# Optimization experiments

Measured on AMD Instinct MI355X. Metric: run time of the kernel, lower is better.

Reference implementation:

```python
import jax, jax.numpy as jnp
import numpy as np

B, H, W, D, C = 2, 16, 16, 16, 128
UNITS = 128
BN_EPS = 1e-3  # keras BatchNormalization default epsilon


def setup_inputs() -> dict:
    key = jax.random.key(0)
    ks = jax.random.split(key, 12)
    lim = np.sqrt(3.0 / C)  # VarianceScaling(1.0, fan_avg, uniform)
    inp = {
        "x": jax.random.normal(ks[0], (B, H, W, D, C), dtype=jnp.float32),
        "gamma": jnp.ones((C,), jnp.float32),
        "beta": jnp.zeros((C,), jnp.float32),
        "moving_mean": jax.random.normal(ks[1], (C,), jnp.float32) * 0.1,
        "moving_var": jnp.ones((C,), jnp.float32) + 0.1 * jax.random.uniform(ks[2], (C,)),
        "Wq": jax.random.uniform(ks[3], (C, UNITS), jnp.float32, -lim, lim),
        "bq": jnp.zeros((UNITS,), jnp.float32),
        "Wk": jax.random.uniform(ks[4], (C, UNITS), jnp.float32, -lim, lim),
        "bk": jnp.zeros((UNITS,), jnp.float32),
        "Wv": jax.random.uniform(ks[5], (C, UNITS), jnp.float32, -lim, lim),
        "bv": jnp.zeros((UNITS,), jnp.float32),
        # proj uses kernel_init(0.0) -> effectively ~0; use tiny scale to keep grads nonzero
        "Wp": jax.random.uniform(ks[6], (UNITS, UNITS), jnp.float32, -1e-5, 1e-5),
        "bp": jnp.zeros((UNITS,), jnp.float32),
    }
    return inp


def reference(x, gamma, beta, moving_mean, moving_var, Wq, bq, Wk, bk, Wv, bv, Wp, bp):
    # BatchNormalization (inference mode): per-channel affine normalization
    xn = (x - moving_mean) * jax.lax.rsqrt(moving_var + BN_EPS) * gamma + beta
    b, h, w, d, c = xn.shape
    n = h * w * d
    scale = jnp.asarray(UNITS, jnp.float32) ** -0.5
    q = (xn @ Wq + bq).reshape(b, n, UNITS)
    k = (xn @ Wk + bk).reshape(b, n, UNITS)
    v = (xn @ Wv + bv).reshape(b, n, UNITS)
    # full self-attention over flattened 3D spatial dims: [b, n, n] scores
    attn = jax.nn.softmax(jnp.einsum('bnc,bmc->bnm', q, k) * scale, axis=-1)
    proj = jnp.einsum('bnm,bmc->bnc', attn, v).reshape(b, h, w, d, UNITS)
    proj = proj @ Wp + bp
    return xn + proj
```

## Files before the change

### kernel.cpp

```cpp
#include <hip/hip_runtime.h>
#include <hip/hip_bf16.h>

using bh8     = __attribute__((ext_vector_type(8))) short;
using floatx4 = __attribute__((ext_vector_type(4))) float;
using uintx2  = __attribute__((ext_vector_type(2))) unsigned;

#define MFMA16 __builtin_amdgcn_mfma_f32_16x16x32_bf16

__device__ __forceinline__ float b2f(short s) {
    union { unsigned u; float f; } v; v.u = ((unsigned)(unsigned short)s) << 16; return v.f;
}
__device__ __forceinline__ short f2b(float f) {
    union { float f; unsigned u; } v; v.f = f;
    unsigned r = (v.u + 0x7fffu + ((v.u >> 16) & 1u)) >> 16;
    return (short)r;
}
__device__ __forceinline__ unsigned pk2(float a, float b) {
    union { __hip_bfloat162 h; unsigned u; } v;
    v.h = __float22bfloat162_rn(make_float2(a, b));
    return v.u;
}
__device__ __forceinline__ float ldf(const void* p, int i, bool f32) {
    return f32 ? ((const float*)p)[i] : b2f(((const short*)p)[i]);
}
__device__ __forceinline__ bool detect_f32(const void* gamma) {
    return ((*(const unsigned*)gamma) & 0xFFFFu) == 0u;
}
__device__ __forceinline__ void gl2lds16(const short* g, short* l) {
    __builtin_amdgcn_global_load_lds(
        (const __attribute__((address_space(1))) void*)g,
        (__attribute__((address_space(3))) void*)l, 16, 0, 0);
}

#define LDW 136

__global__ __launch_bounds__(256) void k_bn_qkv(
    const void* __restrict__ xp,
    const void* __restrict__ gp, const void* __restrict__ bep,
    const void* __restrict__ mmp, const void* __restrict__ mvp,
    const void* __restrict__ Wqp, const void* __restrict__ bqp,
    const void* __restrict__ Wkp, const void* __restrict__ bkp,
    const void* __restrict__ Wvp, const void* __restrict__ bvp,
    short* __restrict__ Qo, short* __restrict__ Ko, short* __restrict__ Vt)
{
    __shared__ float sS[128], sT[128];
    __shared__ __align__(16) short Wt[128 * LDW];
    const bool f32 = detect_f32(gp);
    const int tid = threadIdx.x, wave = tid >> 6, lane = tid & 63;
    const int lq = lane >> 4, lr = lane & 15;
    const int g = blockIdx.x >> 6;
    const int tile = blockIdx.x & 63;
    const int row0 = tile * 128 + wave * 32;

    if (tid < 128) {
        float ga = ldf(gp, tid, f32), be = ldf(bep, tid, f32);
        float mm = ldf(mmp, tid, f32), mv = ldf(mvp, tid, f32);
        float s = ga * rsqrtf(mv + 1e-3f);
        sS[tid] = s;
        sT[tid] = be - mm * s;
    }

    const void* W  = (g == 0) ? Wqp : ((g == 1) ? Wkp : Wvp);
    const void* bb = (g == 0) ? bqp : ((g == 1) ? bkp : bvp);

    if (f32) {
        for (int it = 0; it < 16; ++it) {
            int f = (it * 256 + tid) * 4;
            int c = f >> 7, u = f & 127;
            floatx4 wv = *(const floatx4*)((const float*)W + f);
            #pragma unroll
            for (int jj = 0; jj < 4; ++jj) {
                int j = (jj + (tid >> 1)) & 3;
                Wt[(u + j) * LDW + c] = f2b(wv[j]);
            }
        }
    } else {
        for (int it = 0; it < 8; ++it) {
            int f = (it * 256 + tid) * 8;
            int c = f >> 7, u = f & 127;
            bh8 wv = *(const bh8*)((const short*)W + f);
            #pragma unroll
            for (int jj = 0; jj < 8; ++jj) {
                int j = (jj + tid) & 7;
                Wt[(u + j) * LDW + c] = wv[j];
            }
        }
    }
    __syncthreads();

    bh8 a[2][4];
    #pragma unroll
    for (int rt = 0; rt < 2; ++rt)
        #pragma unroll
        for (int ks = 0; ks < 4; ++ks) {
            int c0 = ks * 32 + lq * 8;
            floatx4 s0 = *(const floatx4*)(&sS[c0]), s1 = *(const floatx4*)(&sS[c0 + 4]);
            floatx4 t0 = *(const floatx4*)(&sT[c0]), t1 = *(const floatx4*)(&sT[c0 + 4]);
            bh8 af;
            if (f32) {
                const float* xr = (const float*)xp + (size_t)(row0 + rt * 16 + lr) * 128 + c0;
                floatx4 x0 = *(const floatx4*)xr, x1 = *(const floatx4*)(xr + 4);
                #pragma unroll
                for (int j = 0; j < 4; ++j) {
                    af[j]     = f2b(x0[j] * s0[j] + t0[j]);
                    af[j + 4] = f2b(x1[j] * s1[j] + t1[j]);
                }
            } else {
                bh8 xv = *(const bh8*)((const short*)xp + (size_t)(row0 + rt * 16 + lr) * 128 + c0);
                #pragma unroll
                for (int j = 0; j < 4; ++j) {
                    af[j]     = f2b(b2f(xv[j]) * s0[j] + t0[j]);
                    af[j + 4] = f2b(b2f(xv[j + 4]) * s1[j] + t1[j]);
                }
            }
            a[rt][ks] = af;
        }

    floatx4 acc[2][8] = {};
    #pragma unroll
    for (int ks = 0; ks < 4; ++ks)
        #pragma unroll
        for (int t = 0; t < 8; ++t) {
            bh8 b = *(const bh8*)(&Wt[(t * 16 + lr) * LDW + ks * 32 + lq * 8]);
            #pragma unroll
            for (int rt = 0; rt < 2; ++rt)
                acc[rt][t] = MFMA16(a[rt][ks], b, acc[rt][t], 0, 0, 0);
        }

    if (g < 2) {
        #pragma unroll
        for (int t = 0; t < 8; ++t) {
            int u = t * 16 + lr;
            float bias = ldf(bb, u, f32);
            #pragma unroll
            for (int rt = 0; rt < 2; ++rt)
                #pragma unroll
                for (int r = 0; r < 4; ++r) {
                    int grow = row0 + rt * 16 + lq * 4 + r;
                    short vb = f2b(acc[rt][t][r] + bias);
                    if (g == 0) Qo[(size_t)grow * 128 + u] = vb;
                    else        Ko[(size_t)grow * 128 + u] = vb;
                }
        }
    } else {
        __syncthreads();
        short* sVt = Wt;
        #pragma unroll
        for (int t = 0; t < 8; ++t) {
            int u = t * 16 + lr;
            float bias = ldf(bb, u, f32);
            #pragma unroll
            for (int rt = 0; rt < 2; ++rt)
                #pragma unroll
                for (int r = 0; r < 4; ++r) {
                    int n = wave * 32 + rt * 16 + lq * 4 + r;
                    sVt[u * LDW + n] = f2b(acc[rt][t][r] + bias);
                }
        }
        __syncthreads();
        int u = tid >> 1, nh = tid & 1;
        int grow0 = tile * 128 + nh * 64;
        int bsb = grow0 >> 12, nn = grow0 & 4095;
        short* dst = Vt + (size_t)bsb * 128 * 4096 + (size_t)u * 4096 + nn;
        #pragma unroll
        for (int j = 0; j < 8; ++j)
            *(bh8*)(dst + j * 8) = *(const bh8*)(&sVt[u * LDW + nh * 64 + j * 8]);
    }
}

#define PLDA 40

__global__ __launch_bounds__(256, 2) void k_attn(
    const short* __restrict__ Qg, const short* __restrict__ Kg,
    const short* __restrict__ Vtg, short* __restrict__ Op,
    float* __restrict__ Lq)
{
    __shared__ __align__(16) short sK[2][32 * 128];
    __shared__ __align__(16) short sV[2][128 * 32];
    __shared__ __align__(16) short sP[4][32 * PLDA];

    const int tid = threadIdx.x, wave = tid >> 6, lane = tid & 63;
    const int lq = lane >> 4, lr = lane & 15;
    const int qt = blockIdx.x >> 3, kq = blockIdx.x & 7;
    const int mq = qt * 128, bs = mq >> 12, key0q = kq * 512;
    const short* Kb = Kg + (size_t)bs * 4096 * 128;
    const short* Vb = Vtg + (size_t)bs * 128 * 4096;
    const int qrow0 = mq + wave * 32;

    bh8 aq[2][4];
    #pragma unroll
    for (int rt = 0; rt < 2; ++rt)
        #pragma unroll
        for (int ks = 0; ks < 4; ++ks)
            aq[rt][ks] = *(const bh8*)(Qg + (size_t)(qrow0 + rt * 16 + lr) * 128 + ks * 32 + lq * 8);

    const int kKey = lane >> 4, kCh = lane & 15;
    const int vU   = lane >> 2, vCh = lane & 3;

    floatx4 accO[2][8] = {};
    float lsum[2] = {};
    const float c2 = 0.12751743f;
    const float m2 = 11.541560f;
    short* Pw = &sP[wave][0];

    #pragma unroll
    for (int rd = 0; rd < 2; ++rd) {
        int key = wave * 8 + rd * 4 + kKey;
        gl2lds16(Kb + (size_t)(key0q + key) * 128 + ((kCh ^ (key & 7)) << 3),
                 &sK[0][(wave * 8 + rd * 4) * 128]);
    }
    #pragma unroll
    for (int rd = 0; rd < 2; ++rd) {
        int u = wave * 32 + rd * 16 + vU;
        gl2lds16(Vb + (size_t)u * 4096 + key0q + ((vCh ^ ((u >> 1) & 3)) << 3),
                 &sV[0][(wave * 32 + rd * 16) * 32]);
    }
    __syncthreads();

    for (int it = 0; it < 16; ++it) {
        const int p = it & 1;
        if (it < 15) {
            const int key1 = key0q + (it + 1) * 32;
            #pragma unroll
            for (int rd = 0; rd < 2; ++rd) {
                int key = wave * 8 + rd * 4 + kKey;
                gl2lds16(Kb + (size_t)(key1 + key) * 128 + ((kCh ^ (key & 7)) << 3),
                         &sK[p ^ 1][(wave * 8 + rd * 4) * 128]);
            }
            #pragma unroll
            for (int rd = 0; rd < 2; ++rd) {
                int u = wave * 32 + rd * 16 + vU;
                gl2lds16(Vb + (size_t)u * 4096 + key1 + ((vCh ^ ((u >> 1) & 3)) << 3),
                         &sV[p ^ 1][(wave * 32 + rd * 16) * 32]);
            }
        }

        const short* sKp = &sK[p][0];
        const short* sVp = &sV[p][0];

        floatx4 s[2][2];
        #pragma unroll
        for (int rt = 0; rt < 2; ++rt)
            #pragma unroll
            for (int t = 0; t < 2; ++t)
                s[rt][t] = floatx4{};
        #pragma unroll
        for (int t = 0; t < 2; ++t)
            #pragma unroll
            for (int ks = 0; ks < 4; ++ks) {
                bh8 kf = *(const bh8*)(&sKp[(t * 16 + lr) * 128 +
                                            (((ks * 4 + lq) ^ (lr & 7)) << 3)]);
                #pragma unroll
                for (int rt = 0; rt < 2; ++rt)
                    s[rt][t] = MFMA16(kf, aq[rt][ks], s[rt][t], 0, 0, 0);
            }

        #pragma unroll
        for (int rt = 0; rt < 2; ++rt)
            #pragma unroll
            for (int t = 0; t < 2; ++t) {
                float e[4];
                #pragma unroll
                for (int r = 0; r < 4; ++r) {
                    e[r] = exp2f(fmaf(s[rt][t][r], c2, -m2));
                    lsum[rt] += e[r];
                }
                uintx2 pw;
                pw[0] = pk2(e[0], e[1]);
                pw[1] = pk2(e[2], e[3]);
                *(uintx2*)(&Pw[(rt * 16 + lr) * PLDA + t * 16 + lq * 4]) = pw;
            }

        bh8 ap[2];
        #pragma unroll
        for (int rt = 0; rt < 2; ++rt)
            ap[rt] = *(const bh8*)(&Pw[(rt * 16 + lr) * PLDA + lq * 8]);

        #pragma unroll
        for (int t = 0; t < 8; ++t) {
            int u = t * 16 + lr;
            bh8 b = *(const bh8*)(&sVp[u * 32 + ((lq ^ ((lr >> 1) & 3)) << 3)]);
            #pragma unroll
            for (int rt = 0; rt < 2; ++rt)
                accO[rt][t] = MFMA16(ap[rt], b, accO[rt][t], 0, 0, 0);
        }
        if (it < 15) __syncthreads();
    }

    #pragma unroll
    for (int rt = 0; rt < 2; ++rt) {
        float v = lsum[rt];
        v += __shfl_xor(v, 16, 64);
        v += __shfl_xor(v, 32, 64);
        if (lane < 16)
            Lq[(size_t)kq * 8192 + qrow0 + rt * 16 + lr] = v;
    }
    short* Ob = Op + (size_t)kq * 8192 * 128;
    #pragma unroll
    for (int rt = 0; rt < 2; ++rt)
        #pragma unroll
        for (int t = 0; t < 8; ++t)
            #pragma unroll
            for (int r = 0; r < 4; ++r)
                Ob[(size_t)(qrow0 + rt * 16 + lq * 4 + r) * 128 + t * 16 + lr]
                    = f2b(accO[rt][t][r]);
}

__global__ __launch_bounds__(256, 2) void k_proj(
    const short* __restrict__ Op, const float* __restrict__ Lq,
    const void* __restrict__ Wpp, const void* __restrict__ bpp,
    const void* __restrict__ xp,
    const void* __restrict__ gp, const void* __restrict__ bep,
    const void* __restrict__ mmp, const void* __restrict__ mvp,
    void* __restrict__ outp)
{
    __shared__ float sS[128], sT[128];
    __shared__ __align__(16) short Wt[128 * LDW];
    __shared__ __align__(16) short sO[16 * LDW];
    const bool f32 = detect_f32(gp);
    const int tid = threadIdx.x, wave = tid >> 6, lane = tid & 63;
    const int lq = lane >> 4, lr = lane & 15;
    const int row0 = blockIdx.x * 16;

    if (tid < 128) {
        float ga = ldf(gp, tid, f32), be = ldf(bep, tid, f32);
        float mm = ldf(mmp, tid, f32), mv = ldf(mvp, tid, f32);
        float s = ga * rsqrtf(mv + 1e-3f);
        sS[tid] = s;
        sT[tid] = be - mm * s;
    }

    if (f32) {
        for (int it = 0; it < 16; ++it) {
            int f = (it * 256 + tid) * 4;
            int c = f >> 7, u = f & 127;
            floatx4 wv = *(const floatx4*)((const float*)Wpp + f);
            #pragma unroll
            for (int jj = 0; jj < 4; ++jj) {
                int j = (jj + (tid >> 1)) & 3;
                Wt[(u + j) * LDW + c] = f2b(wv[j]);
            }
        }
    } else {
        for (int it = 0; it < 8; ++it) {
            int f = (it * 256 + tid) * 8;
            int c = f >> 7, u = f & 127;
            bh8 wv = *(const bh8*)((const short*)Wpp + f);
            #pragma unroll
            for (int jj = 0; jj < 8; ++jj) {
                int j = (jj + tid) & 7;
                Wt[(u + j) * LDW + c] = wv[j];
            }
        }
    }

    {
        int f = tid * 8;
        int row = f >> 7, c = f & 127;
        int grow = row0 + row;
        float L = 0.f;
        #pragma unroll
        for (int w = 0; w < 8; ++w) L += Lq[(size_t)w * 8192 + grow];
        float invL = 1.0f / L;
        float sum[8] = {};
        #pragma unroll
        for (int w = 0; w < 8; ++w) {
            bh8 p = *(const bh8*)(Op + (size_t)w * 8192 * 128 + (size_t)grow * 128 + c);
            #pragma unroll
            for (int j = 0; j < 8; ++j) sum[j] += b2f(p[j]);
        }
        bh8 o;
        #pragma unroll
        for (int j = 0; j < 8; ++j) o[j] = f2b(sum[j] * invL);
        *(bh8*)(&sO[row * LDW + c]) = o;
    }
    __syncthreads();

    bh8 a[4];
    #pragma unroll
    for (int ks = 0; ks < 4; ++ks)
        a[ks] = *(const bh8*)(&sO[lr * LDW + ks * 32 + lq * 8]);

    floatx4 acc[2] = {};
    #pragma unroll
    for (int ks = 0; ks < 4; ++ks)
        #pragma unroll
        for (int tt = 0; tt < 2; ++tt) {
            bh8 b = *(const bh8*)(&Wt[(wave * 32 + tt * 16 + lr) * LDW + ks * 32 + lq * 8]);
            acc[tt] = MFMA16(a[ks], b, acc[tt], 0, 0, 0);
        }

    #pragma unroll
    for (int tt = 0; tt < 2; ++tt) {
        int u = wave * 32 + tt * 16 + lr;
        float bias = ldf(bpp, u, f32);
        float su = sS[u], tu = sT[u];
        #pragma unroll
        for (int r = 0; r < 4; ++r) {
            int grow = row0 + lq * 4 + r;
            float xnv = ldf(xp, grow * 128 + u, f32) * su + tu;
            float v = acc[tt][r] + bias + xnv;
            size_t idx = (size_t)grow * 128 + u;
            if (f32) ((float*)outp)[idx] = v;
            else     ((short*)outp)[idx] = f2b(v);
        }
    }
}

extern "C" void kernel_launch(void* const* d_in, const int* in_sizes, int n_in,
                              void* d_out, int out_size, void* d_ws, size_t ws_size,
                              hipStream_t stream)
{
    const void* x     = d_in[0];
    const void* gamma = d_in[1];
    const void* beta  = d_in[2];
    const void* mmean = d_in[3];
    const void* mvar  = d_in[4];
    const void* Wq    = d_in[5];
    const void* bq    = d_in[6];
    const void* Wk    = d_in[7];
    const void* bk    = d_in[8];
    const void* Wv    = d_in[9];
    const void* bv    = d_in[10];
    const void* Wp    = d_in[11];
    const void* bp    = d_in[12];

    char* ws = (char*)d_ws;
    const size_t MB = 1024u * 1024u;
    short* Q     = (short*)(ws + 0 * MB);
    short* K     = (short*)(ws + 2 * MB);
    short* Vt    = (short*)(ws + 4 * MB);
    short* Opart = (short*)(ws + 6 * MB);
    float* Lsum  = (float*)(ws + 22 * MB);

    k_bn_qkv<<<192, 256, 0, stream>>>(x, gamma, beta, mmean, mvar,
                                      Wq, bq, Wk, bk, Wv, bv, Q, K, Vt);
    k_attn<<<512, 256, 0, stream>>>(Q, K, Vt, Opart, Lsum);
    k_proj<<<512, 256, 0, stream>>>(Opart, Lsum, Wp, bp, x,
                                    gamma, beta, mmean, mvar, d_out);
}
```

Measured before the change: 130.0 us.

## Halve key splits and use 8 waves with 16 query rows each in attention

The attention kernel now uses 512-thread blocks with 8 waves of 16 query rows each, instead of 4 waves of 32 rows, and splits keys 4 ways instead of 8. That halves the grid to 256 blocks, each looping over 1024 keys. Fewer key splits reduce the partial output and sum traffic that the projection kernel must reduce and read. In exchange, each wave does half the MFMA work per K/V tile load, and the grid is smaller, which cuts parallelism and the reuse of K/V fragments per wave.

```diff
diff --git a/kernel.cpp b/kernel.cpp
--- a/kernel.cpp
+++ b/kernel.cpp
@@ -170,140 +170,112 @@
 
 #define PLDA 40
 
-__global__ __launch_bounds__(256, 2) void k_attn(
+__global__ __launch_bounds__(512, 1) void k_attn(
     const short* __restrict__ Qg, const short* __restrict__ Kg,
     const short* __restrict__ Vtg, short* __restrict__ Op,
     float* __restrict__ Lq)
 {
     __shared__ __align__(16) short sK[2][32 * 128];
     __shared__ __align__(16) short sV[2][128 * 32];
-    __shared__ __align__(16) short sP[4][32 * PLDA];
+    __shared__ __align__(16) short sP[8][16 * PLDA];
 
     const int tid = threadIdx.x, wave = tid >> 6, lane = tid & 63;
     const int lq = lane >> 4, lr = lane & 15;
-    const int qt = blockIdx.x >> 3, kq = blockIdx.x & 7;
-    const int mq = qt * 128, bs = mq >> 12, key0q = kq * 512;
+    const int qt = blockIdx.x >> 2, kq = blockIdx.x & 3;
+    const int mq = qt * 128, bs = mq >> 12, key0q = kq * 1024;
     const short* Kb = Kg + (size_t)bs * 4096 * 128;
     const short* Vb = Vtg + (size_t)bs * 128 * 4096;
-    const int qrow0 = mq + wave * 32;
-
-    bh8 aq[2][4];
-    #pragma unroll
-    for (int rt = 0; rt < 2; ++rt)
-        #pragma unroll
-        for (int ks = 0; ks < 4; ++ks)
-            aq[rt][ks] = *(const bh8*)(Qg + (size_t)(qrow0 + rt * 16 + lr) * 128 + ks * 32 + lq * 8);
+    const int qrow0 = mq + wave * 16;
+
+    bh8 aq[4];
+    #pragma unroll
+    for (int ks = 0; ks < 4; ++ks)
+        aq[ks] = *(const bh8*)(Qg + (size_t)(qrow0 + lr) * 128 + ks * 32 + lq * 8);
 
     const int kKey = lane >> 4, kCh = lane & 15;
     const int vU   = lane >> 2, vCh = lane & 3;
 
-    floatx4 accO[2][8] = {};
-    float lsum[2] = {};
+    floatx4 accO[8] = {};
+    float lsum = 0.f;
     const float c2 = 0.12751743f;
     const float m2 = 11.541560f;
     short* Pw = &sP[wave][0];
 
-    #pragma unroll
-    for (int rd = 0; rd < 2; ++rd) {
-        int key = wave * 8 + rd * 4 + kKey;
+    {
+        int key = wave * 4 + kKey;
         gl2lds16(Kb + (size_t)(key0q + key) * 128 + ((kCh ^ (key & 7)) << 3),
-                 &sK[0][(wave * 8 + rd * 4) * 128]);
-    }
-    #pragma unroll
-    for (int rd = 0; rd < 2; ++rd) {
-        int u = wave * 32 + rd * 16 + vU;
+                 &sK[0][(wave * 4) * 128]);
+        int u = wave * 16 + vU;
         gl2lds16(Vb + (size_t)u * 4096 + key0q + ((vCh ^ ((u >> 1) & 3)) << 3),
-                 &sV[0][(wave * 32 + rd * 16) * 32]);
+                 &sV[0][(wave * 16) * 32]);
     }
     __syncthreads();
 
-    for (int it = 0; it < 16; ++it) {
+    for (int it = 0; it < 32; ++it) {
         const int p = it & 1;
-        if (it < 15) {
+        if (it < 31) {
             const int key1 = key0q + (it + 1) * 32;
-            #pragma unroll
-            for (int rd = 0; rd < 2; ++rd) {
-                int key = wave * 8 + rd * 4 + kKey;
-                gl2lds16(Kb + (size_t)(key1 + key) * 128 + ((kCh ^ (key & 7)) << 3),
-                         &sK[p ^ 1][(wave * 8 + rd * 4) * 128]);
-            }
-            #pragma unroll
-            for (int rd = 0; rd < 2; ++rd) {
-                int u = wave * 32 + rd * 16 + vU;
-                gl2lds16(Vb + (size_t)u * 4096 + key1 + ((vCh ^ ((u >> 1) & 3)) << 3),
-                         &sV[p ^ 1][(wave * 32 + rd * 16) * 32]);
-            }
+            int key = wave * 4 + kKey;
+            gl2lds16(Kb + (size_t)(key1 + key) * 128 + ((kCh ^ (key & 7)) << 3),
+                     &sK[p ^ 1][(wave * 4) * 128]);
+            int u = wave * 16 + vU;
+            gl2lds16(Vb + (size_t)u * 4096 + key1 + ((vCh ^ ((u >> 1) & 3)) << 3),
+                     &sV[p ^ 1][(wave * 16) * 32]);
         }
 
         const short* sKp = &sK[p][0];
         const short* sVp = &sV[p][0];
 
-        floatx4 s[2][2];
-        #pragma unroll
-        for (int rt = 0; rt < 2; ++rt)
-            #pragma unroll
-            for (int t = 0; t < 2; ++t)
-                s[rt][t] = floatx4{};
+        floatx4 s[2];
+        s[0] = floatx4{}; s[1] = floatx4{};
         #pragma unroll
         for (int t = 0; t < 2; ++t)
             #pragma unroll
             for (int ks = 0; ks < 4; ++ks) {
                 bh8 kf = *(const bh8*)(&sKp[(t * 16 + lr) * 128 +
                                             (((ks * 4 + lq) ^ (lr & 7)) << 3)]);
-                #pragma unroll
-                for (int rt = 0; rt < 2; ++rt)
-                    s[rt][t] = MFMA16(kf, aq[rt][ks], s[rt][t], 0, 0, 0);
-            }
-
-        #pragma unroll
-        for (int rt = 0; rt < 2; ++rt)
-            #pragma unroll
-            for (int t = 0; t < 2; ++t) {
-                float e[4];
-                #pragma unroll
-                for (int r = 0; r < 4; ++r) {
-                    e[r] = exp2f(fmaf(s[rt][t][r], c2, -m2));
-                    lsum[rt] += e[r];
-                }
-                uintx2 pw;
-                pw[0] = pk2(e[0], e[1]);
-                pw[1] = pk2(e[2], e[3]);
-                *(uintx2*)(&Pw[(rt * 16 + lr) * PLDA + t * 16 + lq * 4]) = pw;
-            }
-
-        bh8 ap[2];
-        #pragma unroll
-        for (int rt = 0; rt < 2; ++rt)
-            ap[rt] = *(const bh8*)(&Pw[(rt * 16 + lr) * PLDA + lq * 8]);
+                s[t] = MFMA16(kf, aq[ks], s[t], 0, 0, 0);
+            }
+
+        #pragma unroll
+        for (int t = 0; t < 2; ++t) {
+            float e[4];
+            #pragma unroll
+            for (int r = 0; r < 4; ++r) {
+                e[r] = exp2f(fmaf(s[t][r], c2, -m2));
+                lsum += e[r];
+            }
+            uintx2 pw;
+            pw[0] = pk2(e[0], e[1]);
+            pw[1] = pk2(e[2], e[3]);
+            *(uintx2*)(&Pw[lr * PLDA + t * 16 + lq * 4]) = pw;
+        }
+
+        bh8 ap = *(const bh8*)(&Pw[lr * PLDA + lq * 8]);
 
         #pragma unroll
         for (int t = 0; t < 8; ++t) {
             int u = t * 16 + lr;
             bh8 b = *(const bh8*)(&sVp[u * 32 + ((lq ^ ((lr >> 1) & 3)) << 3)]);
-            #pragma unroll
-            for (int rt = 0; rt < 2; ++rt)
-                accO[rt][t] = MFMA16(ap[rt], b, accO[rt][t], 0, 0, 0);
-        }
-        if (it < 15) __syncthreads();
-    }
-
-    #pragma unroll
-    for (int rt = 0; rt < 2; ++rt) {
-        float v = lsum[rt];
+            accO[t] = MFMA16(ap, b, accO[t], 0, 0, 0);
+        }
+        if (it < 31) __syncthreads();
+    }
+
+    {
+        float v = lsum;
         v += __shfl_xor(v, 16, 64);
         v += __shfl_xor(v, 32, 64);
         if (lane < 16)
-            Lq[(size_t)kq * 8192 + qrow0 + rt * 16 + lr] = v;
+            Lq[(size_t)kq * 8192 + qrow0 + lr] = v;
     }
     short* Ob = Op + (size_t)kq * 8192 * 128;
     #pragma unroll
-    for (int rt = 0; rt < 2; ++rt)
-        #pragma unroll
-        for (int t = 0; t < 8; ++t)
-            #pragma unroll
-            for (int r = 0; r < 4; ++r)
-                Ob[(size_t)(qrow0 + rt * 16 + lq * 4 + r) * 128 + t * 16 + lr]
-                    = f2b(accO[rt][t][r]);
+    for (int t = 0; t < 8; ++t)
+        #pragma unroll
+        for (int r = 0; r < 4; ++r)
+            Ob[(size_t)(qrow0 + lq * 4 + r) * 128 + t * 16 + lr]
+                = f2b(accO[t][r]);
 }
 
 __global__ __launch_bounds__(256, 2) void k_proj(
@@ -360,11 +332,11 @@
         int grow = row0 + row;
         float L = 0.f;
         #pragma unroll
-        for (int w = 0; w < 8; ++w) L += Lq[(size_t)w * 8192 + grow];
+        for (int w = 0; w < 4; ++w) L += Lq[(size_t)w * 8192 + grow];
         float invL = 1.0f / L;
         float sum[8] = {};
         #pragma unroll
-        for (int w = 0; w < 8; ++w) {
+        for (int w = 0; w < 4; ++w) {
             bh8 p = *(const bh8*)(Op + (size_t)w * 8192 * 128 + (size_t)grow * 128 + c);
             #pragma unroll
             for (int j = 0; j < 8; ++j) sum[j] += b2f(p[j]);
@@ -431,11 +403,11 @@
     short* K     = (short*)(ws + 2 * MB);
     short* Vt    = (short*)(ws + 4 * MB);
     short* Opart = (short*)(ws + 6 * MB);
-    float* Lsum  = (float*)(ws + 22 * MB);
+    float* Lsum  = (float*)(ws + 14 * MB);
 
     k_bn_qkv<<<192, 256, 0, stream>>>(x, gamma, beta, mmean, mvar,
                                       Wq, bq, Wk, bk, Wv, bv, Q, K, Vt);
-    k_attn<<<512, 256, 0, stream>>>(Q, K, Vt, Opart, Lsum);
+    k_attn<<<256, 512, 0, stream>>>(Q, K, Vt, Opart, Lsum);
     k_proj<<<512, 256, 0, stream>>>(Opart, Lsum, Wp, bp, x,
                                     gamma, beta, mmean, mvar, d_out);
 }
```

After: 137.1 us. +5.5%, slower.

## Deepen attention K/V prefetch to four-stage ring with explicit vmcnt waits

Applied to the files above, without the earlier changes.

The attention kernel's K/V staging moves from double buffering to a four-slot LDS ring. Three tiles stay in flight while one is computed, and explicit s_waitcnt vmcnt counts plus raw s_barrier calls replace __syncthreads. The aim is to hide global-to-LDS latency better. In exchange it doubles K/V LDS usage to about 74KB per block, which may reduce occupancy under launch_bounds(256,2), and the hand-tuned wait counts must exactly match the number of loads issued.

```diff
diff --git a/kernel.cpp b/kernel.cpp
--- a/kernel.cpp
+++ b/kernel.cpp
@@ -31,6 +31,9 @@
         (const __attribute__((address_space(1))) void*)g,
         (__attribute__((address_space(3))) void*)l, 16, 0, 0);
 }
+
+#define WAITV(N) do { asm volatile("s_waitcnt vmcnt(" #N ")" ::: "memory"); \
+                      __builtin_amdgcn_sched_barrier(0); } while (0)
 
 #define LDW 136
 
@@ -175,8 +178,8 @@
     const short* __restrict__ Vtg, short* __restrict__ Op,
     float* __restrict__ Lq)
 {
-    __shared__ __align__(16) short sK[2][32 * 128];
-    __shared__ __align__(16) short sV[2][128 * 32];
+    __shared__ __align__(16) short sK[4][32 * 128];
+    __shared__ __align__(16) short sV[4][128 * 32];
     __shared__ __align__(16) short sP[4][32 * PLDA];
 
     const int tid = threadIdx.x, wave = tid >> 6, lane = tid & 63;
@@ -203,40 +206,27 @@
     const float m2 = 11.541560f;
     short* Pw = &sP[wave][0];
 
-    #pragma unroll
-    for (int rd = 0; rd < 2; ++rd) {
-        int key = wave * 8 + rd * 4 + kKey;
-        gl2lds16(Kb + (size_t)(key0q + key) * 128 + ((kCh ^ (key & 7)) << 3),
-                 &sK[0][(wave * 8 + rd * 4) * 128]);
-    }
-    #pragma unroll
-    for (int rd = 0; rd < 2; ++rd) {
-        int u = wave * 32 + rd * 16 + vU;
-        gl2lds16(Vb + (size_t)u * 4096 + key0q + ((vCh ^ ((u >> 1) & 3)) << 3),
-                 &sV[0][(wave * 32 + rd * 16) * 32]);
-    }
-    __syncthreads();
-
-    for (int it = 0; it < 16; ++it) {
-        const int p = it & 1;
-        if (it < 15) {
-            const int key1 = key0q + (it + 1) * 32;
-            #pragma unroll
-            for (int rd = 0; rd < 2; ++rd) {
-                int key = wave * 8 + rd * 4 + kKey;
-                gl2lds16(Kb + (size_t)(key1 + key) * 128 + ((kCh ^ (key & 7)) << 3),
-                         &sK[p ^ 1][(wave * 8 + rd * 4) * 128]);
-            }
-            #pragma unroll
-            for (int rd = 0; rd < 2; ++rd) {
-                int u = wave * 32 + rd * 16 + vU;
-                gl2lds16(Vb + (size_t)u * 4096 + key1 + ((vCh ^ ((u >> 1) & 3)) << 3),
-                         &sV[p ^ 1][(wave * 32 + rd * 16) * 32]);
-            }
-        }
-
-        const short* sKp = &sK[p][0];
-        const short* sVp = &sV[p][0];
+    auto stage = [&](int tt, int bb) {
+        const int key1 = key0q + tt * 32;
+        #pragma unroll
+        for (int rd = 0; rd < 2; ++rd) {
+            int key = wave * 8 + rd * 4 + kKey;
+            gl2lds16(Kb + (size_t)(key1 + key) * 128 + ((kCh ^ (key & 7)) << 3),
+                     &sK[bb][(wave * 8 + rd * 4) * 128]);
+        }
+        #pragma unroll
+        for (int rd = 0; rd < 2; ++rd) {
+            int u = wave * 32 + rd * 16 + vU;
+            gl2lds16(Vb + (size_t)u * 4096 + key1 + ((vCh ^ ((u >> 1) & 3)) << 3),
+                     &sV[bb][(wave * 32 + rd * 16) * 32]);
+        }
+    };
+
+    auto do_tile = [&](int bb) {
+        __builtin_amdgcn_s_barrier();
+        __builtin_amdgcn_sched_barrier(0);
+        const short* sKp = &sK[bb][0];
+        const short* sVp = &sV[bb][0];
 
         floatx4 s[2][2];
         #pragma unroll
@@ -284,8 +274,22 @@
             for (int rt = 0; rt < 2; ++rt)
                 accO[rt][t] = MFMA16(ap[rt], b, accO[rt][t], 0, 0, 0);
         }
-        if (it < 15) __syncthreads();
-    }
+        __builtin_amdgcn_sched_barrier(0);
+        __builtin_amdgcn_s_barrier();
+    };
+
+    stage(0, 0); stage(1, 1); stage(2, 2); stage(3, 3);
+
+    #pragma unroll 4
+    for (int t = 0; t < 12; ++t) {
+        WAITV(12);
+        do_tile(t & 3);
+        stage(t + 4, t & 3);
+    }
+    WAITV(12); do_tile(0);
+    WAITV(8);  do_tile(1);
+    WAITV(4);  do_tile(2);
+    WAITV(0);  do_tile(3);
 
     #pragma unroll
     for (int rt = 0; rt < 2; ++rt) {
```

Measured after the change: 129.4 us. No clear change (-0.5%).
